# Optimization experiments

Measured on AMD Instinct MI355X. Metric: run time of the kernel, lower is better.

## Reference

```python
import jax, jax.numpy as jnp
import numpy as np

NUM_EXPERTS = 64
TOP_K = 2
ALPHA = 0.01


def setup_inputs() -> dict:
    key = jax.random.key(0)
    k1, k2 = jax.random.split(key)
    T, C = 16384, 4096
    x = jax.random.normal(k1, (T, C), dtype=jnp.float32)
    # router weight, init std=0.01 like nn.init.normal_(std=0.01)
    weight = jax.random.normal(k2, (NUM_EXPERTS, C), dtype=jnp.float32) * 0.01
    return {"x": x, "weight": weight}


def reference(x, weight):
    """Top-K softmax gate with load-balancing aux loss (training mode).

    x:      [T, C]
    weight: [E, C]
    Returns (topk_idx [T,K] int32, topk_weight [T,K] f32, aux_loss scalar).
    """
    T = x.shape[0]
    E = weight.shape[0]
    K = TOP_K
    logits = jnp.einsum("tc,ec->te", x.astype(jnp.float32), weight.astype(jnp.float32))  # [T,E]
    scores = jax.nn.softmax(logits, axis=-1)                                             # [T,E]
    topk_weight, topk_idx = jax.lax.top_k(scores, K)                                     # [T,K]
    topk_weight = topk_weight / jnp.sum(topk_weight, axis=-1, keepdims=True)
    # load-balancing aux loss: ce = mean of one-hot over T*K selections
    ce = jnp.zeros((E,), dtype=scores.dtype).at[topk_idx.reshape(-1)].add(1.0) / (T * K)
    fi = ce * E
    Pi = jnp.mean(scores, axis=0)
    aux_loss = jnp.sum(Pi * fi) * ALPHA
    return topk_idx, topk_weight, aux_loss
```

## Files before the change

kernel.cpp:

```cpp
#include <hip/hip_runtime.h>

#define TT 16384
#define CC 4096
#define NE 64
#define TOPK 2
#define ALPHA 0.01f
#define CSPLIT 4
#define KRANGE (CC / CSPLIT)
#define BK 32
#define BT 128
#define NCHUNK (KRANGE / BK)

__global__ __launch_bounds__(256, 2) void gate_gemm(const float* __restrict__ x,
                                                    const float* __restrict__ w,
                                                    float* __restrict__ part) {
    __shared__ float xs[BK][BT + 4];
    __shared__ float wsh[BK][NE + 4];

    const int tile = blockIdx.x;
    const int cs   = blockIdx.y;
    const int t0   = tile * BT;
    const int k0   = cs * KRANGE;
    const int tid  = threadIdx.x;
    const int tg   = tid >> 3;
    const int eg   = tid & 7;
    const int tloc = tg << 2;
    const int e0   = eg << 3;

    float acc[4][8];
#pragma unroll
    for (int i = 0; i < 4; ++i)
#pragma unroll
        for (int j = 0; j < 8; ++j) acc[i][j] = 0.f;

    const float* xb = x + (size_t)t0 * CC + k0;
    const float* wb = w + k0;

    float4 xr[4], wr[2];
#pragma unroll
    for (int it = 0; it < 4; ++it)
        xr[it] = *(const float4*)(xb + (size_t)(tg + 32 * it) * CC + (eg << 2));
#pragma unroll
    for (int it = 0; it < 2; ++it)
        wr[it] = *(const float4*)(wb + (size_t)(tg + 32 * it) * CC + (eg << 2));

    for (int kc = 0; kc < NCHUNK; ++kc) {
        __syncthreads();
#pragma unroll
        for (int it = 0; it < 4; ++it) {
            const int r = tg + 32 * it;
            const int c = eg << 2;
            xs[c + 0][r] = xr[it].x;
            xs[c + 1][r] = xr[it].y;
            xs[c + 2][r] = xr[it].z;
            xs[c + 3][r] = xr[it].w;
        }
#pragma unroll
        for (int it = 0; it < 2; ++it) {
            const int e = tg + 32 * it;
            const int c = eg << 2;
            wsh[c + 0][e] = wr[it].x;
            wsh[c + 1][e] = wr[it].y;
            wsh[c + 2][e] = wr[it].z;
            wsh[c + 3][e] = wr[it].w;
        }
        __syncthreads();
        if (kc + 1 < NCHUNK) {
            const int ko = (kc + 1) * BK;
#pragma unroll
            for (int it = 0; it < 4; ++it)
                xr[it] = *(const float4*)(xb + (size_t)(tg + 32 * it) * CC + ko + (eg << 2));
#pragma unroll
            for (int it = 0; it < 2; ++it)
                wr[it] = *(const float4*)(wb + (size_t)(tg + 32 * it) * CC + ko + (eg << 2));
        }
#pragma unroll
        for (int kk = 0; kk < BK; ++kk) {
            const float4 xa  = *(const float4*)&xs[kk][tloc];
            const float4 wa  = *(const float4*)&wsh[kk][e0];
            const float4 wbv = *(const float4*)&wsh[kk][e0 + 4];
            const float xv[4] = {xa.x, xa.y, xa.z, xa.w};
            const float wv[8] = {wa.x, wa.y, wa.z, wa.w, wbv.x, wbv.y, wbv.z, wbv.w};
#pragma unroll
            for (int i = 0; i < 4; ++i)
#pragma unroll
                for (int j = 0; j < 8; ++j) acc[i][j] = fmaf(xv[i], wv[j], acc[i][j]);
        }
    }

    float* pb = part + (size_t)cs * TT * NE + (size_t)(t0 + tloc) * NE + e0;
#pragma unroll
    for (int i = 0; i < 4; ++i) {
        *(float4*)(pb + (size_t)i * NE)     = make_float4(acc[i][0], acc[i][1], acc[i][2], acc[i][3]);
        *(float4*)(pb + (size_t)i * NE + 4) = make_float4(acc[i][4], acc[i][5], acc[i][6], acc[i][7]);
    }
}

__global__ __launch_bounds__(256) void finalize(const float* __restrict__ part,
                                                float* __restrict__ out,
                                                float* __restrict__ Pacc,
                                                float* __restrict__ Cacc) {
    __shared__ float Ps[NE];
    __shared__ float Csh[NE];
    const int tid = threadIdx.x;
    const int t   = blockIdx.x * 256 + tid;
    if (tid < NE) {
        Ps[tid]  = 0.f;
        Csh[tid] = 0.f;
    }
    __syncthreads();

    float l[NE];
#pragma unroll
    for (int e4 = 0; e4 < 16; ++e4) {
        const float4 v = *(const float4*)(part + (size_t)t * NE + e4 * 4);
        l[e4 * 4 + 0] = v.x;
        l[e4 * 4 + 1] = v.y;
        l[e4 * 4 + 2] = v.z;
        l[e4 * 4 + 3] = v.w;
    }
#pragma unroll
    for (int cs = 1; cs < CSPLIT; ++cs) {
#pragma unroll
        for (int e4 = 0; e4 < 16; ++e4) {
            const float4 v = *(const float4*)(part + (size_t)cs * TT * NE + (size_t)t * NE + e4 * 4);
            l[e4 * 4 + 0] += v.x;
            l[e4 * 4 + 1] += v.y;
            l[e4 * 4 + 2] += v.z;
            l[e4 * 4 + 3] += v.w;
        }
    }

    float m1 = -3.402823466e+38f, m2 = -3.402823466e+38f;
    int   i1 = 0, i2 = 0;
#pragma unroll
    for (int e = 0; e < NE; ++e) {
        const float v = l[e];
        if (v > m1) {
            m2 = m1; i2 = i1;
            m1 = v;  i1 = e;
        } else if (v > m2) {
            m2 = v; i2 = e;
        }
    }

    float s = 0.f;
#pragma unroll
    for (int e = 0; e < NE; ++e) {
        l[e] = expf(l[e] - m1);
        s += l[e];
    }
    const float inv = 1.f / s;

    const int lane = tid & 63;
    float     myP  = 0.f;
#pragma unroll
    for (int e = 0; e < NE; ++e) {
        float r = l[e] * inv;
#pragma unroll
        for (int off = 32; off >= 1; off >>= 1) r += __shfl_xor(r, off, 64);
        if (lane == e) myP = r;
    }
    atomicAdd(&Ps[lane], myP);

    atomicAdd(&Csh[i1], 1.f);
    atomicAdd(&Csh[i2], 1.f);

    const float e2v = expf(m2 - m1);
    const float w1  = 1.f * inv;
    const float w2  = e2v * inv;
    const float iw  = 1.f / (w1 + w2);
    *(float2*)(out + (size_t)t * 2)                  = make_float2((float)i1, (float)i2);
    *(float2*)(out + (size_t)2 * TT + (size_t)t * 2) = make_float2(w1 * iw, w2 * iw);

    __syncthreads();
    if (tid < NE) {
        atomicAdd(&Pacc[tid], Ps[tid]);
        atomicAdd(&Cacc[tid], Csh[tid]);
    }
}

__global__ void auxk(const float* __restrict__ Pacc, const float* __restrict__ Cacc,
                     float* __restrict__ out) {
    const int e  = threadIdx.x;
    const float Pi = Pacc[e] / (float)TT;
    const float fi = Cacc[e] * (float)NE / (float)(TT * TOPK);
    float v = Pi * fi;
#pragma unroll
    for (int off = 32; off >= 1; off >>= 1) v += __shfl_xor(v, off, 64);
    if (e == 0) out[(size_t)2 * TT * 2] = ALPHA * v;
}

extern "C" void kernel_launch(void* const* d_in, const int* in_sizes, int n_in,
                              void* d_out, int out_size, void* d_ws, size_t ws_size,
                              hipStream_t stream) {
    const float* x = (const float*)d_in[0];
    const float* w = (const float*)d_in[1];
    float* out  = (float*)d_out;
    float* part = (float*)d_ws;
    float* Pacc = part + (size_t)CSPLIT * TT * NE;
    float* Cacc = Pacc + NE;

    hipMemsetAsync(Pacc, 0, 2 * NE * sizeof(float), stream);

    dim3 g1(TT / BT, CSPLIT);
    gate_gemm<<<g1, 256, 0, stream>>>(x, w, part);
    finalize<<<TT / 256, 256, 0, stream>>>(part, out, Pacc, Cacc);
    auxk<<<1, 64, 0, stream>>>(Pacc, Cacc, out);
}
```

Measured before the change: 423.5 us.

## Stage GEMM tiles via direct global-to-LDS loads with XOR swizzle and double buffering

Replaces the register-staged transpose into shared memory with __builtin_amdgcn_global_load_lds DMA loads into XOR-swizzled, double-buffered LDS tiles, so the next chunk's load overlaps compute. The inner loop now reads k-contiguous float4 vectors for both x and w, and each thread's token rows become strided by 32. This removes the scalar LDS transpose stores and one barrier per chunk, at the cost of more LDS (double buffering) and correctness relying on the swizzle and wave-layout assumptions of the LDS DMA.

```diff
diff --git a/kernel.cpp b/kernel.cpp
--- a/kernel.cpp
+++ b/kernel.cpp
@@ -11,21 +11,47 @@
 #define BT 128
 #define NCHUNK (KRANGE / BK)
 
+
+__device__ __forceinline__ void stage_chunk(const float* __restrict__ xg,
+                                            const float* __restrict__ wg,
+                                            float* __restrict__ xl,
+                                            float* __restrict__ wl,
+                                            int wv, int ln) {
+#pragma unroll
+    for (int j = 0; j < 4; ++j) {
+        const int r0  = wv * 32 + j * 8;
+        const int row = r0 + (ln >> 3);
+        const float* g = xg + (size_t)row * CC + (((ln & 7) ^ (ln >> 3)) << 2);
+        __builtin_amdgcn_global_load_lds((const __attribute__((address_space(1))) void*)g,
+                                         (__attribute__((address_space(3))) void*)(xl + r0 * 32),
+                                         16, 0, 0);
+    }
+#pragma unroll
+    for (int j = 0; j < 2; ++j) {
+        const int r0  = wv * 16 + j * 8;
+        const int row = r0 + (ln >> 3);
+        const float* g = wg + (size_t)row * CC + (((ln & 7) ^ (wv * 2 + j)) << 2);
+        __builtin_amdgcn_global_load_lds((const __attribute__((address_space(1))) void*)g,
+                                         (__attribute__((address_space(3))) void*)(wl + r0 * 32),
+                                         16, 0, 0);
+    }
+}
+
 __global__ __launch_bounds__(256, 2) void gate_gemm(const float* __restrict__ x,
                                                     const float* __restrict__ w,
                                                     float* __restrict__ part) {
-    __shared__ float xs[BK][BT + 4];
-    __shared__ float wsh[BK][NE + 4];
+    __shared__ float xs[2][BT * BK];
+    __shared__ float ws[2][NE * BK];
 
     const int tile = blockIdx.x;
     const int cs   = blockIdx.y;
     const int t0   = tile * BT;
     const int k0   = cs * KRANGE;
     const int tid  = threadIdx.x;
+    const int wv   = tid >> 6;
+    const int ln   = tid & 63;
     const int tg   = tid >> 3;
     const int eg   = tid & 7;
-    const int tloc = tg << 2;
-    const int e0   = eg << 3;
 
     float acc[4][8];
 #pragma unroll
@@ -36,63 +62,48 @@
     const float* xb = x + (size_t)t0 * CC + k0;
     const float* wb = w + k0;
 
-    float4 xr[4], wr[2];
-#pragma unroll
-    for (int it = 0; it < 4; ++it)
-        xr[it] = *(const float4*)(xb + (size_t)(tg + 32 * it) * CC + (eg << 2));
-#pragma unroll
-    for (int it = 0; it < 2; ++it)
-        wr[it] = *(const float4*)(wb + (size_t)(tg + 32 * it) * CC + (eg << 2));
+    stage_chunk(xb, wb, xs[0], ws[0], wv, ln);
 
     for (int kc = 0; kc < NCHUNK; ++kc) {
-        __syncthreads();
-#pragma unroll
-        for (int it = 0; it < 4; ++it) {
-            const int r = tg + 32 * it;
-            const int c = eg << 2;
-            xs[c + 0][r] = xr[it].x;
-            xs[c + 1][r] = xr[it].y;
-            xs[c + 2][r] = xr[it].z;
-            xs[c + 3][r] = xr[it].w;
+        asm volatile("s_waitcnt vmcnt(0)" ::: "memory");
+        __builtin_amdgcn_s_barrier();
+        __builtin_amdgcn_sched_barrier(0);
+
+        if (kc + 1 < NCHUNK)
+            stage_chunk(xb + (kc + 1) * BK, wb + (kc + 1) * BK,
+                        xs[(kc + 1) & 1], ws[(kc + 1) & 1], wv, ln);
+
+        const float* __restrict__ xbuf = xs[kc & 1];
+        const float* __restrict__ wbuf = ws[kc & 1];
+
+#pragma unroll
+        for (int kq = 0; kq < 8; ++kq) {
+            float4 xq[4];
+            const int xsw = ((kq ^ (tg & 7)) << 2);
+#pragma unroll
+            for (int i = 0; i < 4; ++i)
+                xq[i] = *(const float4*)&xbuf[(tg + 32 * i) * BK + xsw];
+            const int wsw = ((kq ^ eg) << 2);
+#pragma unroll
+            for (int j = 0; j < 8; ++j) {
+                const float4 wq = *(const float4*)&wbuf[(eg * 8 + j) * BK + wsw];
+#pragma unroll
+                for (int i = 0; i < 4; ++i) {
+                    acc[i][j] = fmaf(xq[i].x, wq.x, acc[i][j]);
+                    acc[i][j] = fmaf(xq[i].y, wq.y, acc[i][j]);
+                    acc[i][j] = fmaf(xq[i].z, wq.z, acc[i][j]);
+                    acc[i][j] = fmaf(xq[i].w, wq.w, acc[i][j]);
+                }
+            }
         }
-#pragma unroll
-        for (int it = 0; it < 2; ++it) {
-            const int e = tg + 32 * it;
-            const int c = eg << 2;
-            wsh[c + 0][e] = wr[it].x;
-            wsh[c + 1][e] = wr[it].y;
-            wsh[c + 2][e] = wr[it].z;
-            wsh[c + 3][e] = wr[it].w;
-        }
-        __syncthreads();
-        if (kc + 1 < NCHUNK) {
-            const int ko = (kc + 1) * BK;
-#pragma unroll
-            for (int it = 0; it < 4; ++it)
-                xr[it] = *(const float4*)(xb + (size_t)(tg + 32 * it) * CC + ko + (eg << 2));
-#pragma unroll
-            for (int it = 0; it < 2; ++it)
-                wr[it] = *(const float4*)(wb + (size_t)(tg + 32 * it) * CC + ko + (eg << 2));
-        }
-#pragma unroll
-        for (int kk = 0; kk < BK; ++kk) {
-            const float4 xa  = *(const float4*)&xs[kk][tloc];
-            const float4 wa  = *(const float4*)&wsh[kk][e0];
-            const float4 wbv = *(const float4*)&wsh[kk][e0 + 4];
-            const float xv[4] = {xa.x, xa.y, xa.z, xa.w};
-            const float wv[8] = {wa.x, wa.y, wa.z, wa.w, wbv.x, wbv.y, wbv.z, wbv.w};
-#pragma unroll
-            for (int i = 0; i < 4; ++i)
-#pragma unroll
-                for (int j = 0; j < 8; ++j) acc[i][j] = fmaf(xv[i], wv[j], acc[i][j]);
-        }
-    }
-
-    float* pb = part + (size_t)cs * TT * NE + (size_t)(t0 + tloc) * NE + e0;
+    }
+
+    const int e0 = eg * 8;
 #pragma unroll
     for (int i = 0; i < 4; ++i) {
-        *(float4*)(pb + (size_t)i * NE)     = make_float4(acc[i][0], acc[i][1], acc[i][2], acc[i][3]);
-        *(float4*)(pb + (size_t)i * NE + 4) = make_float4(acc[i][4], acc[i][5], acc[i][6], acc[i][7]);
+        float* pb = part + (size_t)cs * TT * NE + (size_t)(t0 + tg + 32 * i) * NE + e0;
+        *(float4*)(pb)     = make_float4(acc[i][0], acc[i][1], acc[i][2], acc[i][3]);
+        *(float4*)(pb + 4) = make_float4(acc[i][4], acc[i][5], acc[i][6], acc[i][7]);
     }
 }
 
```

New measurement: 438.6 us. +3.5%, slower.
